# Kernel tuning notes

Measured on AMD Instinct MI355X. Metric: run time of the kernel, lower is better.

## Reference

```python
import jax, jax.numpy as jnp
import numpy as np

NUM_POINTS = 4_000_000
RADIUS = 2.5
IMG = 1024


def setup_inputs() -> dict:
    key = jax.random.key(0)
    k1, k2, k3, k4 = jax.random.split(key, 4)
    # Uniform sampling inside a sphere, mirroring the torch __init__
    phi = jax.random.uniform(k1, (NUM_POINTS,)) * 2 * np.pi
    costheta = jax.random.uniform(k2, (NUM_POINTS,)) * 2 - 1
    u = jax.random.uniform(k3, (NUM_POINTS,))
    theta = jnp.arccos(costheta)
    r = RADIUS * u ** (1.0 / 3.0)
    x = r * jnp.sin(theta) * jnp.cos(phi)
    y = r * jnp.sin(theta) * jnp.sin(phi)
    z = r * jnp.cos(theta)
    positions = jnp.stack([x, y, z], axis=-1).astype(jnp.float32)  # [N,3]
    colors = jax.random.uniform(k4, (NUM_POINTS, 3), dtype=jnp.float32)
    # Camera at origin looking down +z, points translated to z in [2.5, 7.5]
    camera_pose = jnp.eye(4, dtype=jnp.float32).at[2, 3].set(5.0)
    intrinsics = jnp.array([[800.0, 0.0, 512.0],
                            [0.0, 800.0, 512.0],
                            [0.0, 0.0, 1.0]], dtype=jnp.float32)
    return {"positions": positions, "colors": colors,
            "camera_pose": camera_pose, "intrinsics": intrinsics,
            "H": IMG, "W": IMG}


def reference(positions, colors, camera_pose, intrinsics, H, W):
    # points_cam = (R @ P^T)^T + t^T
    R = camera_pose[:3, :3]
    t = camera_pose[:3, 3]
    pc = positions @ R.T + t  # [N,3]
    x, y, z = pc[:, 0], pc[:, 1], pc[:, 2]
    fx, fy = intrinsics[0, 0], intrinsics[1, 1]
    cx, cy = intrinsics[0, 2], intrinsics[1, 2]
    u = fx * x / z + cx
    v = fy * y / z + cy
    # int() truncation toward zero, matching the torch loop
    xi = u.astype(jnp.int32)
    yi = v.astype(jnp.int32)
    valid = (xi >= 0) & (xi < W) & (yi >= 0) & (yi < H)
    n = positions.shape[0]
    pix = jnp.where(valid, yi * W + xi, H * W)  # invalid -> sentinel segment
    winner = jax.ops.segment_max(jnp.arange(n, dtype=jnp.int32), pix,
                                 num_segments=H * W + 1)[: H * W]
    has = winner >= 0  # empty segments get iinfo(int32).min
    img_flat = jnp.where(has[:, None],
                         colors[jnp.clip(winner, 0, n - 1)],
                         jnp.float32(0.0))  # [H*W, 3]
    img = img_flat.reshape(H, W, 3).transpose(2, 0, 1)[None]  # [1,3,H,W]
    return jnp.clip(img, 0.0, 1.0)
```

## Files before the change

kernel.cpp:

```cpp
#include <hip/hip_runtime.h>


#define NB      1024
#define TB      512
#define TBP     1024
#define NT      1024
#define GP      4
#define NG      (NT / GP)
#define PPB_MAX 4096
#define IMGW    1024
#define IMGHW   (1024 * 1024)

__host__ __device__ __forceinline__ unsigned align8u(unsigned x) {
    return (x + 7u) & ~7u;
}

__global__ void __launch_bounds__(TB)
binsort_kernel(const float* __restrict__ pos,
               const float* __restrict__ pose,
               const float* __restrict__ intr,
               unsigned* __restrict__ bins,
               unsigned* __restrict__ histG,
               int n, int ppb, int region) {
    __shared__ unsigned stash[PPB_MAX];
    __shared__ unsigned h[NT];
    __shared__ unsigned base_[NT];
    __shared__ unsigned cur[NT];
    __shared__ unsigned sc[TB];

    int tid = threadIdx.x;
    for (int t = tid; t < NT; t += TB) h[t] = 0;
    __syncthreads();

    float r00 = pose[0], r01 = pose[1], r02 = pose[2],  t0 = pose[3];
    float r10 = pose[4], r11 = pose[5], r12 = pose[6],  t1 = pose[7];
    float r20 = pose[8], r21 = pose[9], r22 = pose[10], t2 = pose[11];
    float fx = intr[0], cx = intr[2];
    float fy = intr[4], cy = intr[5];

    int start = blockIdx.x * ppb;
    int cnt = min(start + ppb, n) - start;
    if (cnt < 0) cnt = 0;

    const float4* p4 = (const float4*)(pos + (size_t)3 * (size_t)start);
    for (int j4 = tid * 4; j4 < cnt; j4 += TB * 4) {
        int g = j4 >> 2;
        float4 A = p4[3 * g + 0];
        float4 B = p4[3 * g + 1];
        float4 C = p4[3 * g + 2];
        float xs0 = A.x, ys0 = A.y, zs0 = A.z;
        float xs1 = A.w, ys1 = B.x, zs1 = B.y;
        float xs2 = B.z, ys2 = B.w, zs2 = C.x;
        float xs3 = C.y, ys3 = C.z, zs3 = C.w;

        unsigned pv[4];
        #define PROJ(K, PX, PY, PZ)                                          \
        {                                                                    \
            float x = r00 * PX + r01 * PY + r02 * PZ + t0;                   \
            float y = r10 * PX + r11 * PY + r12 * PZ + t1;                   \
            float z = r20 * PX + r21 * PY + r22 * PZ + t2;                   \
            float u = fx * x / z + cx;                                       \
            float v = fy * y / z + cy;                                       \
            int xi = (int)u;                                                 \
            int yi = (int)v;                                                 \
            unsigned p = 0xFFFFFFFFu;                                        \
            if (xi >= 0 && xi < IMGW && yi >= 0 && yi < IMGW) {              \
                p = ((unsigned)yi << 10) | (unsigned)xi;                     \
                int tt = ((yi >> 5) << 5) + (xi >> 5);                       \
                atomicAdd(&h[tt], 1u);                                       \
            }                                                                \
            pv[K] = p;                                                       \
        }
        PROJ(0, xs0, ys0, zs0)
        PROJ(1, xs1, ys1, zs1)
        PROJ(2, xs2, ys2, zs2)
        PROJ(3, xs3, ys3, zs3)
        #undef PROJ

        *(uint4*)&stash[j4] = make_uint4(pv[0], pv[1], pv[2], pv[3]);
    }
    __syncthreads();

    unsigned c0 = h[2 * tid];
    unsigned c1 = h[2 * tid + 1];
    unsigned v = c0 + c1;
    sc[tid] = v;
    __syncthreads();
    for (int off = 1; off < TB; off <<= 1) {
        unsigned add = (tid >= off) ? sc[tid - off] : 0u;
        __syncthreads();
        v += add;
        sc[tid] = v;
        __syncthreads();
    }
    base_[2 * tid]     = v - c0 - c1;
    base_[2 * tid + 1] = v - c1;
    __syncthreads();

    for (int t = tid; t < NT; t += TB) {
        cur[t] = base_[t];
        histG[(size_t)blockIdx.x * NT + t] = (base_[t] << 16) | h[t];
    }
    __syncthreads();

    unsigned* myRegion = bins + (size_t)blockIdx.x * (size_t)region;
    for (int j = tid; j < cnt; j += TB) {
        unsigned pv = stash[j];
        if (pv == 0xFFFFFFFFu) continue;
        unsigned xi = pv & 1023u, yi = pv >> 10;
        unsigned t  = ((yi >> 5) << 5) + (xi >> 5);
        unsigned lp = ((yi & 31u) << 5) + (xi & 31u);
        unsigned slot = atomicAdd(&cur[t], 1u);
        myRegion[slot] = (lp << 22) | (unsigned)(start + j);
    }
}

__global__ void __launch_bounds__(TBP)
paint_kernel(const unsigned* __restrict__ bins,
             const unsigned* __restrict__ histG,
             const float* __restrict__ colors,
             float* __restrict__ out,
             int region) {
    __shared__ unsigned win[GP * 1024];
    int g = blockIdx.x;
    int tid = threadIdx.x;
    #pragma unroll
    for (int l = tid; l < GP * 1024; l += TBP) win[l] = 0;
    __syncthreads();

    {
        const unsigned* hg = histG + (size_t)tid * NT + g * GP;
        unsigned pk0 = hg[0], pk1 = hg[1], pk2 = hg[2], pk3 = hg[3];
        unsigned c[GP] = {pk0 & 0xFFFFu, pk1 & 0xFFFFu,
                          pk2 & 0xFFFFu, pk3 & 0xFFFFu};
        const unsigned* p = bins + (size_t)tid * (size_t)region + (pk0 >> 16);
        #pragma unroll
        for (int s = 0; s < GP; ++s) {
            for (unsigned k = 0; k < c[s]; ++k) {
                unsigned e = *p++;
                atomicMax(&win[(s << 10) + (e >> 22)],
                          (e & 0x3FFFFFu) + 1u);
            }
        }
    }
    __syncthreads();

    int tx0 = ((g * GP) & 31) << 5;
    int ty0 = ((g * GP) >> 5) << 5;
    for (int l = tid; l < GP * 1024; l += TBP) {
        int lx = l & 127, ly = l >> 7;
        int s = lx >> 5, col = lx & 31;
        unsigned w = win[(s << 10) + (ly << 5) + col];
        float r = 0.0f, gc = 0.0f, bl = 0.0f;
        if (w) {
            unsigned wi = w - 1u;
            r  = fminf(fmaxf(colors[3 * wi + 0], 0.0f), 1.0f);
            gc = fminf(fmaxf(colors[3 * wi + 1], 0.0f), 1.0f);
            bl = fminf(fmaxf(colors[3 * wi + 2], 0.0f), 1.0f);
        }
        int p = (ty0 + ly) * IMGW + tx0 + lx;
        out[p] = r;
        out[IMGHW + p] = gc;
        out[2 * IMGHW + p] = bl;
    }
}


__global__ void proj_simple(const float* __restrict__ pos,
                            const float* __restrict__ pose,
                            const float* __restrict__ intr,
                            const int* __restrict__ Hp,
                            const int* __restrict__ Wp,
                            int* __restrict__ winner, int n) {
    int i = blockIdx.x * blockDim.x + threadIdx.x;
    if (i >= n) return;
    float px = pos[3 * i], py = pos[3 * i + 1], pz = pos[3 * i + 2];
    float x = pose[0] * px + pose[1] * py + pose[2]  * pz + pose[3];
    float y = pose[4] * px + pose[5] * py + pose[6]  * pz + pose[7];
    float z = pose[8] * px + pose[9] * py + pose[10] * pz + pose[11];
    float u = intr[0] * x / z + intr[2];
    float v = intr[4] * y / z + intr[5];
    int xi = (int)u, yi = (int)v;
    int W = *Wp, H = *Hp;
    if (xi >= 0 && xi < W && yi >= 0 && yi < H) atomicMax(&winner[yi * W + xi], i);
}

__global__ void paint_simple(const int* __restrict__ winner,
                             const float* __restrict__ colors,
                             float* __restrict__ out, int HW) {
    int p = blockIdx.x * blockDim.x + threadIdx.x;
    if (p >= HW) return;
    int w = winner[p];
    float r = 0.0f, g = 0.0f, b = 0.0f;
    if (w >= 0) {
        r = fminf(fmaxf(colors[3 * w + 0], 0.0f), 1.0f);
        g = fminf(fmaxf(colors[3 * w + 1], 0.0f), 1.0f);
        b = fminf(fmaxf(colors[3 * w + 2], 0.0f), 1.0f);
    }
    out[p] = r; out[HW + p] = g; out[2 * HW + p] = b;
}

extern "C" void kernel_launch(void* const* d_in, const int* in_sizes, int n_in,
                              void* d_out, int out_size, void* d_ws, size_t ws_size,
                              hipStream_t stream) {
    const float* positions = (const float*)d_in[0];
    const float* colors    = (const float*)d_in[1];
    const float* pose      = (const float*)d_in[2];
    const float* intr      = (const float*)d_in[3];
    const int*   Hp        = (const int*)d_in[4];
    const int*   Wp        = (const int*)d_in[5];
    float* out = (float*)d_out;

    int n  = in_sizes[0] / 3;
    int HW = out_size / 3;

    int ppb = ((n + NB - 1) / NB + 3) & ~3;
    int region = (int)align8u((unsigned)ppb);
    unsigned* bins  = (unsigned*)d_ws;
    unsigned* histG = bins + (size_t)NB * (size_t)region;
    size_t needFast = ((size_t)NB * region + (size_t)NB * NT) * sizeof(unsigned);

    bool fast = (HW == IMGHW) && (n >= 4096) && ((n & 3) == 0) &&
                (ppb <= PPB_MAX) && (n <= 4000000) && (ws_size >= needFast);

    if (fast) {
        binsort_kernel<<<NB, TB, 0, stream>>>(positions, pose, intr,
                                              bins, histG, n, ppb, region);
        paint_kernel<<<NG, TBP, 0, stream>>>(bins, histG, colors, out, region);
        return;
    }

    int* winner = (int*)d_ws;
    const int block = 256;
    hipMemsetAsync(winner, 0xFF, (size_t)HW * sizeof(int), stream);
    int grid = (n + block - 1) / block;
    proj_simple<<<grid, block, 0, stream>>>(positions, pose, intr, Hp, Wp,
                                            winner, n);
    int grid2 = (HW + block - 1) / block;
    paint_simple<<<grid2, block, 0, stream>>>(winner, colors, out, HW);
}
```

Baseline: 71.34 us.

## Transpose histogram layout and read bin segments cooperatively per wavefront

The histogram is now written group-major, so each paint block loads its 1024 packed headers as one contiguous uint4 stream into shared memory. The paint loop also changes: instead of each thread walking one source block's variable-length segment serially, each wavefront takes one source block and its 64 lanes read the four tile segments together, giving coalesced reads and balanced work. The tile index is recovered from prefix counts. The cost is extra shared memory for the headers and a strided scatter when the histogram is written.

```diff
diff --git a/kernel.cpp b/kernel.cpp
--- a/kernel.cpp
+++ b/kernel.cpp
@@ -99,7 +99,8 @@
 
     for (int t = tid; t < NT; t += TB) {
         cur[t] = base_[t];
-        histG[(size_t)blockIdx.x * NT + t] = (base_[t] << 16) | h[t];
+        histG[(size_t)(t >> 2) * (NB * 4) + (blockIdx.x << 2) + (t & 3)] =
+            (base_[t] << 16) | h[t];
     }
     __syncthreads();
 
@@ -121,26 +122,28 @@
              const float* __restrict__ colors,
              float* __restrict__ out,
              int region) {
+    __shared__ uint4    hgs[NB];
     __shared__ unsigned win[GP * 1024];
     int g = blockIdx.x;
     int tid = threadIdx.x;
+
+    hgs[tid] = ((const uint4*)histG)[((size_t)g << 10) + tid];
     #pragma unroll
     for (int l = tid; l < GP * 1024; l += TBP) win[l] = 0;
     __syncthreads();
 
-    {
-        const unsigned* hg = histG + (size_t)tid * NT + g * GP;
-        unsigned pk0 = hg[0], pk1 = hg[1], pk2 = hg[2], pk3 = hg[3];
-        unsigned c[GP] = {pk0 & 0xFFFFu, pk1 & 0xFFFFu,
-                          pk2 & 0xFFFFu, pk3 & 0xFFFFu};
-        const unsigned* p = bins + (size_t)tid * (size_t)region + (pk0 >> 16);
-        #pragma unroll
-        for (int s = 0; s < GP; ++s) {
-            for (unsigned k = 0; k < c[s]; ++k) {
-                unsigned e = *p++;
-                atomicMax(&win[(s << 10) + (e >> 22)],
-                          (e & 0x3FFFFFu) + 1u);
-            }
+    int wave = tid >> 6, lane = tid & 63;
+    for (int b = wave; b < NB; b += (TBP / 64)) {
+        uint4 pk = hgs[b];
+        unsigned c0 = pk.x & 0xFFFFu, c1 = pk.y & 0xFFFFu;
+        unsigned c2 = pk.z & 0xFFFFu, c3 = pk.w & 0xFFFFu;
+        unsigned b01 = c0 + c1, b012 = b01 + c2;
+        unsigned total = b012 + c3;
+        const unsigned* p = bins + (size_t)b * (size_t)region + (pk.x >> 16);
+        for (unsigned k = lane; k < total; k += 64) {
+            unsigned e = p[k];
+            unsigned s = (k >= c0) + (k >= b01) + (k >= b012);
+            atomicMax(&win[(s << 10) + (e >> 22)], (e & 0x3FFFFFu) + 1u);
         }
     }
     __syncthreads();
```

After: 71.74 us. No clear change (+0.6%).
